# Optimization experiments

Hardware: AMD Instinct MI355X
Metric: run time of the kernel (lower is better)

Reference implementation:

```python
import jax, jax.numpy as jnp
import numpy as np
from jax import lax

MIN_TRACK_LEN = 20

def setup_inputs() -> dict:
    key = jax.random.key(0)
    k1, k2 = jax.random.split(key)
    B, F, T, NB = 16, 257, 8000, 64
    mag = jax.random.uniform(k1, (B, F, T), dtype=jnp.float32)          # magnitude spectrogram, >= 0
    freq_fb = jax.random.uniform(k2, (NB, F), dtype=jnp.float32)        # band filterbank
    return {
        "mag": mag,
        "freq_fb": freq_fb,
        "noise_scale": jnp.array(1.5, dtype=jnp.float32),
        "raw_rise": jnp.array(-1.5, dtype=jnp.float32),
        "raw_fall": jnp.array(-3.0, dtype=jnp.float32),
    }

def reference(mag, freq_fb, noise_scale, raw_rise, raw_fall):
    rise = jax.nn.sigmoid(raw_rise)
    fall = jax.nn.sigmoid(raw_fall)
    T = mag.shape[2]
    # initial noise floor from first min_track_len frames: (B, F)
    init_min = jnp.clip(jnp.min(mag[:, :, :min(MIN_TRACK_LEN, T)], axis=2), 1e-5, None)
    floor_min = init_min * 0.5

    def step(noise_floor, frame):  # noise_floor, frame: (B, F)
        alpha = jnp.where(frame > noise_floor, rise, fall)
        nf = (1.0 - alpha) * noise_floor + alpha * frame
        nf = jnp.maximum(nf, floor_min)
        return nf, nf

    _, noise_t = lax.scan(step, init_min, jnp.moveaxis(mag, 2, 0))  # (T, B, F)
    running_noise = jnp.moveaxis(noise_t, 0, 2)                      # (B, F, T)

    vnr = mag / (jnp.abs(noise_scale) * running_noise + 1e-8)        # (B, F, T)
    vnr_bands = jnp.tanh(jnp.einsum('nf,bft->bnt', freq_fb, vnr) / 10.0)
    return jnp.nan_to_num(vnr_bands, nan=0.0, posinf=1.0, neginf=0.0)
```

## Files before the change

### kernel.cpp

```cpp
#include <hip/hip_runtime.h>
#include <stdint.h>

#define B_      16
#define F_      257
#define T_      8000
#define NB_     64
#define TT_     64
#define NTILES  125
#define TPC     2
#define NCHUNK  64
#define WTILES  2

typedef __attribute__((ext_vector_type(8))) short short8;
typedef __attribute__((ext_vector_type(4))) float floatx4;

__device__ __forceinline__ unsigned short f2bf(float x) {
    union { float f; unsigned u; } v; v.f = x;
    unsigned r = v.u + 0x7FFFu + ((v.u >> 16) & 1u);
    return (unsigned short)(r >> 16);
}
__device__ __forceinline__ float bf2f(unsigned short h) {
    union { float f; unsigned u; } v; v.u = ((unsigned)h) << 16;
    return v.f;
}

__device__ __forceinline__ int stidx(int t, int f) {
    const int st = ((t & 3) << 2) | ((t >> 2) & 3);
    return t * 256 + (f ^ (st << 3));
}

__global__ __launch_bounds__(256, 4) void vnr_fused_kernel(
    const float* __restrict__ mag, const float* __restrict__ fb,
    const float* __restrict__ p_ns, const float* __restrict__ p_rr,
    const float* __restrict__ p_rf, float* __restrict__ out)
{
    __shared__ unsigned short tile16[64 * 256];
    __shared__ float mag256s[64];
    __shared__ float vnr256s[64];

    const int tid  = threadIdx.x;
    const int lane = tid & 63;
    const int w    = tid >> 6;
    const int l15  = tid & 15;
    const int q    = (tid & 63) >> 4;

    const int bid = blockIdx.x;
    const int b   = bid & 15;
    const int c   = bid >> 4;

    const float ns   = fabsf(p_ns[0]);
    const float rise = 1.0f / (1.0f + __expf(-p_rr[0]));
    const float fall = 1.0f / (1.0f + __expf(-p_rf[0]));

    const float* magp = mag + (size_t)b * (size_t)F_ * (size_t)T_;

    short8 afrag[8];
    {
        const float* fbrow = fb + (16 * w + l15) * F_;
        #pragma unroll
        for (int kt = 0; kt < 8; ++kt) {
            const int f0 = 32 * kt + 8 * q;
            short8 a;
            #pragma unroll
            for (int j = 0; j < 8; ++j) a[j] = (short)f2bf(fbrow[f0 + j]);
            afrag[kt] = a;
        }
    }
    float fb256[4];
    #pragma unroll
    for (int r = 0; r < 4; ++r) fb256[r] = fb[(16 * w + 4 * q + r) * F_ + 256];

    const int f_own = tid;
    float mn = 1e30f;
    #pragma unroll
    for (int t = 0; t < 20; ++t) mn = fminf(mn, magp[(size_t)f_own * T_ + t]);
    const float initv  = fmaxf(mn, 1e-5f);
    const float floorv = 0.5f * initv;
    float nf = initv;

    float nf256 = 0.f, floor256 = 0.f;
    if (tid == 0) {
        float m2 = 1e30f;
        for (int t = 0; t < 20; ++t) m2 = fminf(m2, magp[(size_t)256 * T_ + t]);
        float iv = fmaxf(m2, 1e-5f);
        nf256 = iv; floor256 = 0.5f * iv;
    }

    const int bodyBeg = TPC * c;
    const int tileBeg = (c == 0) ? 0 : max(0, bodyBeg - WTILES);
    const int tileEnd = min(bodyBeg + TPC, NTILES);

    for (int tile = tileBeg; tile < tileEnd; ++tile) {
        const bool body = (tile >= bodyBeg);
        const int t0 = tile * TT_;

        __syncthreads();
        #pragma unroll 4
        for (int i = 0; i < 8; ++i) {
            const int p = i * 16 + (tid >> 4);
            const int s = tid & 15;
            const float4 ga = *(const float4*)&magp[(size_t)(2 * p)     * T_ + (t0 + 4 * s)];
            const float4 gb = *(const float4*)&magp[(size_t)(2 * p + 1) * T_ + (t0 + 4 * s)];
            #pragma unroll
            for (int k = 0; k < 4; ++k) {
                const int t = 4 * s + k;
                const float xa = (&ga.x)[k];
                const float xb = (&gb.x)[k];
                const unsigned pack = (unsigned)f2bf(xa) | ((unsigned)f2bf(xb) << 16);
                *(unsigned*)&tile16[stidx(t, 2 * p)] = pack;
            }
        }
        if (w == 0) mag256s[lane] = magp[(size_t)256 * T_ + (t0 + lane)];
        __syncthreads();

        {
            float nfl = nf;
            if (body) {
                #pragma unroll
                for (int jb = 0; jb < 64; jb += 16) {
                    unsigned short xs[16];
                    #pragma unroll
                    for (int u = 0; u < 16; ++u)
                        xs[u] = tile16[stidx(jb + u, f_own)];
                    #pragma unroll
                    for (int u = 0; u < 16; ++u) {
                        const float x = bf2f(xs[u]);
                        const float a = (x > nfl) ? rise : fall;
                        nfl = fmaxf(__builtin_fmaf(a, x - nfl, nfl), floorv);
                        const float vnr = x * __builtin_amdgcn_rcpf(ns * nfl + 1e-8f);
                        tile16[stidx(jb + u, f_own)] = f2bf(vnr);
                    }
                }
            } else {
                #pragma unroll
                for (int jb = 0; jb < 64; jb += 16) {
                    unsigned short xs[16];
                    #pragma unroll
                    for (int u = 0; u < 16; ++u)
                        xs[u] = tile16[stidx(jb + u, f_own)];
                    #pragma unroll
                    for (int u = 0; u < 16; ++u) {
                        const float x = bf2f(xs[u]);
                        const float a = (x > nfl) ? rise : fall;
                        nfl = fmaxf(__builtin_fmaf(a, x - nfl, nfl), floorv);
                    }
                }
            }
            nf = nfl;
            if (tid == 0) {
                float nl = nf256;
                for (int j = 0; j < 64; ++j) {
                    const float x = mag256s[j];
                    const float a = (x > nl) ? rise : fall;
                    nl = fmaxf(__builtin_fmaf(a, x - nl, nl), floor256);
                    if (body) vnr256s[j] = x * __builtin_amdgcn_rcpf(ns * nl + 1e-8f);
                }
                nf256 = nl;
            }
        }
        if (!body) continue;
        __syncthreads();

        const int stl3 = ((((l15 & 3) << 2) | (l15 >> 2)) << 3);
        floatx4 acc[4];
        #pragma unroll
        for (int tt = 0; tt < 4; ++tt) acc[tt] = (floatx4){0.f, 0.f, 0.f, 0.f};

        #pragma unroll
        for (int kt = 0; kt < 8; ++kt) {
            #pragma unroll
            for (int tt = 0; tt < 4; ++tt) {
                const int t = tt * 16 + l15;
                const short8* bp = (const short8*)
                    &tile16[t * 256 + ((32 * kt + 8 * q) ^ stl3)];
                acc[tt] = __builtin_amdgcn_mfma_f32_16x16x32_bf16(afrag[kt], *bp, acc[tt], 0, 0, 0);
            }
        }

        const size_t outb = (size_t)b * NB_ * T_;
        #pragma unroll
        for (int tt = 0; tt < 4; ++tt) {
            const int t = tt * 16 + l15;
            const float v256 = vnr256s[t];
            #pragma unroll
            for (int r = 0; r < 4; ++r) {
                const float s = acc[tt][r] + fb256[r] * v256;
                const float e = __expf(s * 0.2f);
                const float y = 1.0f - 2.0f * __builtin_amdgcn_rcpf(e + 1.0f);
                out[outb + (size_t)(16 * w + 4 * q + r) * T_ + (size_t)(t0 + t)] = y;
            }
        }
    }
}

extern "C" void kernel_launch(void* const* d_in, const int* in_sizes, int n_in,
                              void* d_out, int out_size, void* d_ws, size_t ws_size,
                              hipStream_t stream) {
    (void)in_sizes; (void)n_in; (void)d_ws; (void)ws_size; (void)out_size;
    const float* mag = (const float*)d_in[0];
    const float* fb  = (const float*)d_in[1];
    const float* ns  = (const float*)d_in[2];
    const float* rr  = (const float*)d_in[3];
    const float* rf  = (const float*)d_in[4];
    float* out = (float*)d_out;

    dim3 grid(B_ * NCHUNK);
    dim3 block(256);
    hipLaunchKernelGGL(vnr_fused_kernel, grid, block, 0, stream, mag, fb, ns, rr, rf, out);
}
```

Measured before the change: 249.9 us.

## Prefetch next tile into registers and overlap loads with the recurrence scan

```diff
diff --git a/kernel.cpp b/kernel.cpp
--- a/kernel.cpp
+++ b/kernel.cpp
@@ -8,20 +8,25 @@
 #define TT_     64
 #define NTILES  125
 #define TPC     2
-#define NCHUNK  64
+#define NCHUNK  63
 #define WTILES  2
 
 typedef __attribute__((ext_vector_type(8))) short short8;
 typedef __attribute__((ext_vector_type(4))) float floatx4;
 
-__device__ __forceinline__ unsigned short f2bf(float x) {
-    union { float f; unsigned u; } v; v.f = x;
-    unsigned r = v.u + 0x7FFFu + ((v.u >> 16) & 1u);
+__device__ __forceinline__ unsigned fbits(float x) {
+    union { float f; unsigned u; } v; v.f = x; return v.u;
+}
+__device__ __forceinline__ float bf2f(unsigned short h) {
+    union { float f; unsigned u; } v; v.u = ((unsigned)h) << 16; return v.f;
+}
+__device__ __forceinline__ unsigned short f2bf_rne(float x) {
+    unsigned u = fbits(x);
+    unsigned r = u + 0x7FFFu + ((u >> 16) & 1u);
     return (unsigned short)(r >> 16);
 }
-__device__ __forceinline__ float bf2f(unsigned short h) {
-    union { float f; unsigned u; } v; v.u = ((unsigned)h) << 16;
-    return v.f;
+__device__ __forceinline__ unsigned packbf(float a, float b) {
+    return __builtin_amdgcn_perm(fbits(b), fbits(a), 0x07060302u);
 }
 
 __device__ __forceinline__ int stidx(int t, int f) {
@@ -43,6 +48,8 @@
     const int w    = tid >> 6;
     const int l15  = tid & 15;
     const int q    = (tid & 63) >> 4;
+    const int s    = tid & 15;
+    const int rq   = (tid >> 4) & 3;
 
     const int bid = blockIdx.x;
     const int b   = bid & 15;
@@ -62,7 +69,7 @@
             const int f0 = 32 * kt + 8 * q;
             short8 a;
             #pragma unroll
-            for (int j = 0; j < 8; ++j) a[j] = (short)f2bf(fbrow[f0 + j]);
+            for (int j = 0; j < 8; ++j) a[j] = (short)f2bf_rne(fbrow[f0 + j]);
             afrag[kt] = a;
         }
     }
@@ -90,74 +97,116 @@
     const int tileBeg = (c == 0) ? 0 : max(0, bodyBeg - WTILES);
     const int tileEnd = min(bodyBeg + TPC, NTILES);
 
+    float4   ld[8];
+    unsigned pk[16];
+    const int fw = 64 * w + 4 * rq;
+
+    #define ISSUE_AB(pbase, t0n)                                              \
+        _Pragma("unroll")                                                     \
+        for (int p = 0; p < 2; ++p)                                           \
+            _Pragma("unroll")                                                 \
+            for (int r = 0; r < 4; ++r)                                       \
+                ld[p * 4 + r] = *(const float4*)&magp[                        \
+                    (size_t)(fw + 16 * (p + (pbase)) + r) * T_ + (t0n) + 4 * s];
+
+    #define PACK_A()                                                          \
+        _Pragma("unroll")                                                     \
+        for (int p = 0; p < 2; ++p)                                           \
+            _Pragma("unroll")                                                 \
+            for (int k = 0; k < 4; ++k) {                                     \
+                pk[p * 8 + k * 2 + 0] = packbf(ld[p * 4 + 0][k], ld[p * 4 + 1][k]); \
+                pk[p * 8 + k * 2 + 1] = packbf(ld[p * 4 + 2][k], ld[p * 4 + 3][k]); \
+            }
+
+    {
+        const int t0f = tileBeg * TT_;
+        ISSUE_AB(0, t0f);
+        PACK_A();
+        ISSUE_AB(2, t0f);
+    }
+
     for (int tile = tileBeg; tile < tileEnd; ++tile) {
         const bool body = (tile >= bodyBeg);
-        const int t0 = tile * TT_;
-
-        __syncthreads();
-        #pragma unroll 4
-        for (int i = 0; i < 8; ++i) {
-            const int p = i * 16 + (tid >> 4);
-            const int s = tid & 15;
-            const float4 ga = *(const float4*)&magp[(size_t)(2 * p)     * T_ + (t0 + 4 * s)];
-            const float4 gb = *(const float4*)&magp[(size_t)(2 * p + 1) * T_ + (t0 + 4 * s)];
+        const int t0  = tile * TT_;
+        const int t0n = min(tile + 1, tileEnd - 1) * TT_;
+
+        #pragma unroll
+        for (int p = 0; p < 2; ++p)
             #pragma unroll
             for (int k = 0; k < 4; ++k) {
-                const int t = 4 * s + k;
-                const float xa = (&ga.x)[k];
-                const float xb = (&gb.x)[k];
-                const unsigned pack = (unsigned)f2bf(xa) | ((unsigned)f2bf(xb) << 16);
-                *(unsigned*)&tile16[stidx(t, 2 * p)] = pack;
-            }
-        }
+                const int idx = stidx(4 * s + k, fw + 16 * p);
+                *(uint2*)&tile16[idx] = make_uint2(pk[p * 8 + k * 2], pk[p * 8 + k * 2 + 1]);
+            }
+        #pragma unroll
+        for (int p = 0; p < 2; ++p)
+            #pragma unroll
+            for (int k = 0; k < 4; ++k) {
+                const unsigned lo = packbf(ld[p * 4 + 0][k], ld[p * 4 + 1][k]);
+                const unsigned hi = packbf(ld[p * 4 + 2][k], ld[p * 4 + 3][k]);
+                const int idx = stidx(4 * s + k, fw + 16 * (p + 2));
+                *(uint2*)&tile16[idx] = make_uint2(lo, hi);
+            }
         if (w == 0) mag256s[lane] = magp[(size_t)256 * T_ + (t0 + lane)];
-        __syncthreads();
+
+        ISSUE_AB(0, t0n);
 
         {
             float nfl = nf;
-            if (body) {
-                #pragma unroll
-                for (int jb = 0; jb < 64; jb += 16) {
-                    unsigned short xs[16];
+            unsigned short xs[2][16];
+            #pragma unroll
+            for (int u = 0; u < 16; ++u) xs[0][u] = tile16[stidx(u, f_own)];
+            #pragma unroll
+            for (int jb = 0; jb < 64; jb += 16) {
+                const int cur = (jb >> 4) & 1;
+                if (jb + 16 < 64) {
                     #pragma unroll
                     for (int u = 0; u < 16; ++u)
-                        xs[u] = tile16[stidx(jb + u, f_own)];
+                        xs[cur ^ 1][u] = tile16[stidx(jb + 16 + u, f_own)];
+                }
+                if (body) {
                     #pragma unroll
                     for (int u = 0; u < 16; ++u) {
-                        const float x = bf2f(xs[u]);
+                        const float x = bf2f(xs[cur][u]);
                         const float a = (x > nfl) ? rise : fall;
                         nfl = fmaxf(__builtin_fmaf(a, x - nfl, nfl), floorv);
-                        const float vnr = x * __builtin_amdgcn_rcpf(ns * nfl + 1e-8f);
-                        tile16[stidx(jb + u, f_own)] = f2bf(vnr);
+                        const float vnr = x * __builtin_amdgcn_rcpf(
+                                              __builtin_fmaf(ns, nfl, 1e-8f));
+                        tile16[stidx(jb + u, f_own)] =
+                            (unsigned short)(fbits(vnr) >> 16);
                     }
-                }
-            } else {
-                #pragma unroll
-                for (int jb = 0; jb < 64; jb += 16) {
-                    unsigned short xs[16];
-                    #pragma unroll
-                    for (int u = 0; u < 16; ++u)
-                        xs[u] = tile16[stidx(jb + u, f_own)];
+                } else {
                     #pragma unroll
                     for (int u = 0; u < 16; ++u) {
-                        const float x = bf2f(xs[u]);
+                        const float x = bf2f(xs[cur][u]);
                         const float a = (x > nfl) ? rise : fall;
                         nfl = fmaxf(__builtin_fmaf(a, x - nfl, nfl), floorv);
                     }
                 }
             }
             nf = nfl;
-            if (tid == 0) {
-                float nl = nf256;
-                for (int j = 0; j < 64; ++j) {
-                    const float x = mag256s[j];
+        }
+        if (tid == 0) {
+            float nl = nf256;
+            #pragma unroll
+            for (int jb = 0; jb < 64; jb += 16) {
+                float m[16];
+                #pragma unroll
+                for (int u = 0; u < 16; ++u) m[u] = mag256s[jb + u];
+                #pragma unroll
+                for (int u = 0; u < 16; ++u) {
+                    const float x = m[u];
                     const float a = (x > nl) ? rise : fall;
                     nl = fmaxf(__builtin_fmaf(a, x - nl, nl), floor256);
-                    if (body) vnr256s[j] = x * __builtin_amdgcn_rcpf(ns * nl + 1e-8f);
+                    if (body) vnr256s[jb + u] =
+                        x * __builtin_amdgcn_rcpf(__builtin_fmaf(ns, nl, 1e-8f));
                 }
-                nf256 = nl;
-            }
-        }
+            }
+            nf256 = nl;
+        }
+
+        PACK_A();
+        ISSUE_AB(2, t0n);
+
         if (!body) continue;
         __syncthreads();
 
@@ -165,7 +214,6 @@
         floatx4 acc[4];
         #pragma unroll
         for (int tt = 0; tt < 4; ++tt) acc[tt] = (floatx4){0.f, 0.f, 0.f, 0.f};
-
         #pragma unroll
         for (int kt = 0; kt < 8; ++kt) {
             #pragma unroll
@@ -184,13 +232,16 @@
             const float v256 = vnr256s[t];
             #pragma unroll
             for (int r = 0; r < 4; ++r) {
-                const float s = acc[tt][r] + fb256[r] * v256;
-                const float e = __expf(s * 0.2f);
+                const float sv = acc[tt][r] + fb256[r] * v256;
+                const float e = __expf(sv * 0.2f);
                 const float y = 1.0f - 2.0f * __builtin_amdgcn_rcpf(e + 1.0f);
                 out[outb + (size_t)(16 * w + 4 * q + r) * T_ + (size_t)(t0 + t)] = y;
             }
         }
-    }
+        __syncthreads();
+    }
+    #undef ISSUE_AB
+    #undef PACK_A
 }
 
 extern "C" void kernel_launch(void* const* d_in, const int* in_sizes, int n_in,
@@ -199,12 +250,12 @@
     (void)in_sizes; (void)n_in; (void)d_ws; (void)ws_size; (void)out_size;
     const float* mag = (const float*)d_in[0];
     const float* fb  = (const float*)d_in[1];
-    const float* ns  = (const float*)d_in[2];
+    const float* nsp = (const float*)d_in[2];
     const float* rr  = (const float*)d_in[3];
     const float* rf  = (const float*)d_in[4];
-    float* out = (float*)d_out;
+    float* outp = (float*)d_out;
 
     dim3 grid(B_ * NCHUNK);
     dim3 block(256);
-    hipLaunchKernelGGL(vnr_fused_kernel, grid, block, 0, stream, mag, fb, ns, rr, rf, out);
-}
+    hipLaunchKernelGGL(vnr_fused_kernel, grid, block, 0, stream, mag, fb, nsp, rr, rf, outp);
+}
```

New measurement: 278.3 us. +11.3%, slower.

## Stage mag rows in padded f-major LDS and make the noise recurrence branchless

Applied to the files above, without the earlier changes.

```diff
diff --git a/kernel.cpp b/kernel.cpp
--- a/kernel.cpp
+++ b/kernel.cpp
@@ -8,34 +8,40 @@
 #define TT_     64
 #define NTILES  125
 #define TPC     2
-#define NCHUNK  64
+#define NCHUNK  63
 #define WTILES  2
+#define LDW     72
 
 typedef __attribute__((ext_vector_type(8))) short short8;
 typedef __attribute__((ext_vector_type(4))) float floatx4;
 
-__device__ __forceinline__ unsigned short f2bf(float x) {
-    union { float f; unsigned u; } v; v.f = x;
-    unsigned r = v.u + 0x7FFFu + ((v.u >> 16) & 1u);
+__device__ __forceinline__ unsigned fbits(float x) {
+    union { float f; unsigned u; } v; v.f = x; return v.u;
+}
+__device__ __forceinline__ float ubits(unsigned u) {
+    union { float f; unsigned u; } v; v.u = u; return v.f;
+}
+__device__ __forceinline__ unsigned short f2bf_rne(float x) {
+    unsigned u = fbits(x);
+    unsigned r = u + 0x7FFFu + ((u >> 16) & 1u);
     return (unsigned short)(r >> 16);
 }
-__device__ __forceinline__ float bf2f(unsigned short h) {
-    union { float f; unsigned u; } v; v.u = ((unsigned)h) << 16;
-    return v.f;
+__device__ __forceinline__ unsigned packbf(float a, float b) {
+    return __builtin_amdgcn_perm(fbits(b), fbits(a), 0x07060302u);
 }
 
 __device__ __forceinline__ int stidx(int t, int f) {
     const int st = ((t & 3) << 2) | ((t >> 2) & 3);
     return t * 256 + (f ^ (st << 3));
 }
+
 
 __global__ __launch_bounds__(256, 4) void vnr_fused_kernel(
     const float* __restrict__ mag, const float* __restrict__ fb,
     const float* __restrict__ p_ns, const float* __restrict__ p_rr,
     const float* __restrict__ p_rf, float* __restrict__ out)
 {
-    __shared__ unsigned short tile16[64 * 256];
-    __shared__ float mag256s[64];
+    __shared__ unsigned short lds[F_ * LDW];
     __shared__ float vnr256s[64];
 
     const int tid  = threadIdx.x;
@@ -43,6 +49,8 @@
     const int w    = tid >> 6;
     const int l15  = tid & 15;
     const int q    = (tid & 63) >> 4;
+    const int fr2  = lane >> 4;
+    const int tq   = lane & 15;
 
     const int bid = blockIdx.x;
     const int b   = bid & 15;
@@ -62,7 +70,7 @@
             const int f0 = 32 * kt + 8 * q;
             short8 a;
             #pragma unroll
-            for (int j = 0; j < 8; ++j) a[j] = (short)f2bf(fbrow[f0 + j]);
+            for (int j = 0; j < 8; ++j) a[j] = (short)f2bf_rne(fbrow[f0 + j]);
             afrag[kt] = a;
         }
     }
@@ -90,74 +98,75 @@
     const int tileBeg = (c == 0) ? 0 : max(0, bodyBeg - WTILES);
     const int tileEnd = min(bodyBeg + TPC, NTILES);
 
+    bool prevBody = false;
     for (int tile = tileBeg; tile < tileEnd; ++tile) {
         const bool body = (tile >= bodyBeg);
         const int t0 = tile * TT_;
 
-        __syncthreads();
-        #pragma unroll 4
-        for (int i = 0; i < 8; ++i) {
-            const int p = i * 16 + (tid >> 4);
-            const int s = tid & 15;
-            const float4 ga = *(const float4*)&magp[(size_t)(2 * p)     * T_ + (t0 + 4 * s)];
-            const float4 gb = *(const float4*)&magp[(size_t)(2 * p + 1) * T_ + (t0 + 4 * s)];
-            #pragma unroll
-            for (int k = 0; k < 4; ++k) {
-                const int t = 4 * s + k;
-                const float xa = (&ga.x)[k];
-                const float xb = (&gb.x)[k];
-                const unsigned pack = (unsigned)f2bf(xa) | ((unsigned)f2bf(xb) << 16);
-                *(unsigned*)&tile16[stidx(t, 2 * p)] = pack;
-            }
-        }
-        if (w == 0) mag256s[lane] = magp[(size_t)256 * T_ + (t0 + lane)];
-        __syncthreads();
+        if (prevBody) __syncthreads();
+
+        #pragma unroll
+        for (int i = 0; i < 16; ++i) {
+            const int f = 64 * w + 4 * i + fr2;
+            const float4 g = *(const float4*)&magp[(size_t)f * T_ + (t0 + 4 * tq)];
+            const unsigned lo = packbf(g.x, g.y);
+            const unsigned hi = packbf(g.z, g.w);
+            *(uint2*)&lds[LDW * f + 4 * tq] = make_uint2(lo, hi);
+        }
+        if (tid < 16) {
+            const float4 g = *(const float4*)&magp[(size_t)256 * T_ + (t0 + 4 * tid)];
+            *(uint2*)&lds[LDW * 256 + 4 * tid] = make_uint2(packbf(g.x, g.y), packbf(g.z, g.w));
+        }
+
+        uint4 rv[8];
+        #pragma unroll
+        for (int j = 0; j < 8; ++j)
+            rv[j] = *(const uint4*)&lds[LDW * f_own + 8 * j];
+
+        if (body) __syncthreads();
 
         {
             float nfl = nf;
-            if (body) {
+            #pragma unroll
+            for (int j = 0; j < 64; ++j) {
+                const unsigned uu = ((const unsigned*)rv)[j >> 1];
+                const float x = ubits((j & 1) ? (uu & 0xFFFF0000u) : (uu << 16));
+                const float d = x - nfl;
+                const float yr = __builtin_fmaf(rise, d, nfl);
+                const float yf = __builtin_fmaf(fall, d, nfl);
+                nfl = fmaxf(fmaxf(yr, yf), floorv);
+                if (body) {
+                    const float vnr = x * __builtin_amdgcn_rcpf(
+                                          __builtin_fmaf(ns, nfl, 1e-8f));
+                    lds[stidx(j, f_own)] = (unsigned short)(fbits(vnr) >> 16);
+                }
+            }
+            nf = nfl;
+        }
+        if (tid == 0) {
+            float nl = nf256;
+            #pragma unroll
+            for (int h = 0; h < 2; ++h) {
+                uint4 rh[4];
                 #pragma unroll
-                for (int jb = 0; jb < 64; jb += 16) {
-                    unsigned short xs[16];
-                    #pragma unroll
-                    for (int u = 0; u < 16; ++u)
-                        xs[u] = tile16[stidx(jb + u, f_own)];
-                    #pragma unroll
-                    for (int u = 0; u < 16; ++u) {
-                        const float x = bf2f(xs[u]);
-                        const float a = (x > nfl) ? rise : fall;
-                        nfl = fmaxf(__builtin_fmaf(a, x - nfl, nfl), floorv);
-                        const float vnr = x * __builtin_amdgcn_rcpf(ns * nfl + 1e-8f);
-                        tile16[stidx(jb + u, f_own)] = f2bf(vnr);
-                    }
+                for (int j = 0; j < 4; ++j)
+                    rh[j] = *(const uint4*)&lds[LDW * 256 + 32 * h + 8 * j];
+                #pragma unroll
+                for (int u = 0; u < 32; ++u) {
+                    const unsigned uu = ((const unsigned*)rh)[u >> 1];
+                    const float x = ubits((u & 1) ? (uu & 0xFFFF0000u) : (uu << 16));
+                    const float d = x - nl;
+                    const float yr = __builtin_fmaf(rise, d, nl);
+                    const float yf = __builtin_fmaf(fall, d, nl);
+                    nl = fmaxf(fmaxf(yr, yf), floor256);
+                    if (body) vnr256s[32 * h + u] =
+                        x * __builtin_amdgcn_rcpf(__builtin_fmaf(ns, nl, 1e-8f));
                 }
-            } else {
-                #pragma unroll
-                for (int jb = 0; jb < 64; jb += 16) {
-                    unsigned short xs[16];
-                    #pragma unroll
-                    for (int u = 0; u < 16; ++u)
-                        xs[u] = tile16[stidx(jb + u, f_own)];
-                    #pragma unroll
-                    for (int u = 0; u < 16; ++u) {
-                        const float x = bf2f(xs[u]);
-                        const float a = (x > nfl) ? rise : fall;
-                        nfl = fmaxf(__builtin_fmaf(a, x - nfl, nfl), floorv);
-                    }
-                }
-            }
-            nf = nfl;
-            if (tid == 0) {
-                float nl = nf256;
-                for (int j = 0; j < 64; ++j) {
-                    const float x = mag256s[j];
-                    const float a = (x > nl) ? rise : fall;
-                    nl = fmaxf(__builtin_fmaf(a, x - nl, nl), floor256);
-                    if (body) vnr256s[j] = x * __builtin_amdgcn_rcpf(ns * nl + 1e-8f);
-                }
-                nf256 = nl;
-            }
-        }
+            }
+            nf256 = nl;
+        }
+
+        prevBody = body;
         if (!body) continue;
         __syncthreads();
 
@@ -165,14 +174,13 @@
         floatx4 acc[4];
         #pragma unroll
         for (int tt = 0; tt < 4; ++tt) acc[tt] = (floatx4){0.f, 0.f, 0.f, 0.f};
-
         #pragma unroll
         for (int kt = 0; kt < 8; ++kt) {
             #pragma unroll
             for (int tt = 0; tt < 4; ++tt) {
                 const int t = tt * 16 + l15;
                 const short8* bp = (const short8*)
-                    &tile16[t * 256 + ((32 * kt + 8 * q) ^ stl3)];
+                    &lds[t * 256 + ((32 * kt + 8 * q) ^ stl3)];
                 acc[tt] = __builtin_amdgcn_mfma_f32_16x16x32_bf16(afrag[kt], *bp, acc[tt], 0, 0, 0);
             }
         }
@@ -184,8 +192,8 @@
             const float v256 = vnr256s[t];
             #pragma unroll
             for (int r = 0; r < 4; ++r) {
-                const float s = acc[tt][r] + fb256[r] * v256;
-                const float e = __expf(s * 0.2f);
+                const float sv = acc[tt][r] + fb256[r] * v256;
+                const float e = __expf(sv * 0.2f);
                 const float y = 1.0f - 2.0f * __builtin_amdgcn_rcpf(e + 1.0f);
                 out[outb + (size_t)(16 * w + 4 * q + r) * T_ + (size_t)(t0 + t)] = y;
             }
@@ -198,13 +206,13 @@
                               hipStream_t stream) {
     (void)in_sizes; (void)n_in; (void)d_ws; (void)ws_size; (void)out_size;
     const float* mag = (const float*)d_in[0];
-    const float* fb  = (const float*)d_in[1];
-    const float* ns  = (const float*)d_in[2];
+    const float* fbp = (const float*)d_in[1];
+    const float* nsp = (const float*)d_in[2];
     const float* rr  = (const float*)d_in[3];
     const float* rf  = (const float*)d_in[4];
-    float* out = (float*)d_out;
+    float* outp = (float*)d_out;
 
     dim3 grid(B_ * NCHUNK);
     dim3 block(256);
-    hipLaunchKernelGGL(vnr_fused_kernel, grid, block, 0, stream, mag, fb, ns, rr, rf, out);
-}
+    hipLaunchKernelGGL(vnr_fused_kernel, grid, block, 0, stream, mag, fbp, nsp, rr, rf, outp);
+}
```

Measured after the change: 254.1 us. No clear change (+1.7%).
